# Performance work log

Measured on AMD Instinct MI355X. Metric: run time of the kernel, lower is better.

Reference implementation:

```python
import jax, jax.numpy as jnp
import numpy as np

N_QUBITS = 6
N_LAYERS = 4
N_ACTIONS = 4
PRE_DIM = 64
BATCH = 262144


def _cnot(state, ctrl, tgt):
    # state: (B, 2,...,2); flip target axis on the control=1 slice
    ca, ta = 1 + ctrl, 1 + tgt
    s0 = jnp.take(state, 0, axis=ca)
    s1 = jnp.take(state, 1, axis=ca)
    ta_in = ta if ta < ca else ta - 1
    s1 = jnp.flip(s1, axis=ta_in)
    return jnp.stack([s0, s1], axis=ca)


def _ry_batched(state, angles_q, q):
    # angles_q: (B,) per-sample RY angle on qubit q (AngleEmbedding)
    h = angles_q * 0.5
    c, s = jnp.cos(h), jnp.sin(h)
    R = jnp.stack([jnp.stack([c, -s], -1), jnp.stack([s, c], -1)], -2)  # (B,2,2)
    st = jnp.moveaxis(state, 1 + q, -1)
    st = jnp.einsum('b...i,bji->b...j', st, R)
    return jnp.moveaxis(st, -1, 1 + q)


def _ry_scalar(state, theta, q):
    h = theta * 0.5
    c, s = jnp.cos(h), jnp.sin(h)
    R = jnp.stack([jnp.stack([c, -s]), jnp.stack([s, c])])  # (2,2)
    st = jnp.moveaxis(state, 1 + q, -1)
    st = st @ R.T  # new_j = sum_i R[j,i] amp_i
    return jnp.moveaxis(st, -1, 1 + q)


def _circuit(xp, qw):
    # xp: (B, n_qubits) angles; qw: (n_layers, n_qubits)
    B = xp.shape[0]
    state = jnp.zeros((B,) + (2,) * N_QUBITS, xp.dtype)
    state = state.at[(slice(None),) + (0,) * N_QUBITS].set(1.0)
    for q in range(N_QUBITS):
        state = _ry_batched(state, xp[:, q], q)
    for l in range(N_LAYERS):
        for i in range(N_QUBITS):
            state = _cnot(state, i, (i + 1) % N_QUBITS)
        for i in range(N_QUBITS):
            state = _ry_scalar(state, qw[l, i], i)
    probs = state * state  # RY/CNOT are real; state stays real
    all_axes = tuple(range(1, N_QUBITS + 1))
    zs = []
    for q in range(N_QUBITS):
        p = jnp.sum(probs, axis=tuple(a for a in all_axes if a != 1 + q))  # (B,2)
        zs.append(p[:, 0] - p[:, 1])
    return jnp.stack(zs, -1)  # (B, n_qubits)


def setup_inputs() -> dict:
    key = jax.random.key(0)
    ks = jax.random.split(key, 10)
    x = jax.random.normal(ks[0], (BATCH, N_QUBITS), jnp.float32)
    sc = 1.0 / np.sqrt(N_QUBITS)
    W1 = jax.random.uniform(ks[1], (PRE_DIM, N_QUBITS), jnp.float32, -sc, sc)
    b1 = jax.random.uniform(ks[2], (PRE_DIM,), jnp.float32, -sc, sc)
    sc2 = 1.0 / np.sqrt(PRE_DIM)
    W2 = jax.random.uniform(ks[3], (N_QUBITS, PRE_DIM), jnp.float32, -sc2, sc2)
    b2 = jax.random.uniform(ks[4], (N_QUBITS,), jnp.float32, -sc2, sc2)
    qw = jax.random.uniform(ks[5], (N_LAYERS, N_QUBITS), jnp.float32, 0.0, 2.0 * np.pi)
    Wp = jax.random.uniform(ks[6], (N_ACTIONS, N_QUBITS), jnp.float32, -sc, sc)
    bp = jax.random.uniform(ks[7], (N_ACTIONS,), jnp.float32, -sc, sc)
    Wv = jax.random.uniform(ks[8], (1, N_QUBITS), jnp.float32, -sc, sc)
    bv = jax.random.uniform(ks[9], (1,), jnp.float32, -sc, sc)
    return {"x": x, "W1": W1, "b1": b1, "W2": W2, "b2": b2, "qw": qw,
            "Wp": Wp, "bp": bp, "Wv": Wv, "bv": bv}


def reference(x, W1, b1, W2, b2, qw, Wp, bp, Wv, bv):
    h = jax.nn.relu(x @ W1.T + b1)
    xp = jax.nn.relu(h @ W2.T + b2)          # (B, n_qubits)
    qout = _circuit(xp, qw)                   # (B, n_qubits)
    policy = jax.nn.softmax(qout @ Wp.T + bp, axis=-1)
    value = (qout @ Wv.T + bv)[:, 0]
    return policy, value
```

## Files before the change

kernel.cpp:

```cpp
#include <hip/hip_runtime.h>
#include <math.h>


#define NQ 6
#define NL 4
#define NA 4
#define PD 64
#define NS 64

__global__ __launch_bounds__(256) void qpolicy_kernel(
    const float* __restrict__ x,
    const float* __restrict__ W1,
    const float* __restrict__ b1,
    const float* __restrict__ W2,
    const float* __restrict__ b2,
    const float* __restrict__ qw,
    const float* __restrict__ Wp,
    const float* __restrict__ bp,
    const float* __restrict__ Wv,
    const float* __restrict__ bv,
    float* __restrict__ out,
    int B)
{
    const int tid = blockIdx.x * blockDim.x + threadIdx.x;

    float xi[NQ];
    {
        const float2* xv = reinterpret_cast<const float2*>(x + (size_t)tid * NQ);
        float2 a = xv[0], b = xv[1], c = xv[2];
        xi[0] = a.x; xi[1] = a.y; xi[2] = b.x; xi[3] = b.y; xi[4] = c.x; xi[5] = c.y;
    }

    float h[PD];
#pragma unroll
    for (int j = 0; j < PD; ++j) {
        float acc = b1[j];
#pragma unroll
        for (int q = 0; q < NQ; ++q) acc = fmaf(xi[q], W1[j * NQ + q], acc);
        h[j] = fmaxf(acc, 0.0f);
    }

    float xp[NQ];
#pragma unroll
    for (int i = 0; i < NQ; ++i) {
        float acc = b2[i];
#pragma unroll
        for (int j = 0; j < PD; ++j) acc = fmaf(h[j], W2[i * PD + j], acc);
        xp[i] = fmaxf(acc, 0.0f);
    }

    float cq[NQ], sq[NQ];
#pragma unroll
    for (int q = 0; q < NQ; ++q) {
        __sincosf(0.5f * xp[q], &sq[q], &cq[q]);
    }
    float st[NS];
    st[0] = 1.0f;
#pragma unroll
    for (int q = 0; q < NQ; ++q) {
        const int sz = 1 << q;
#pragma unroll
        for (int k = sz - 1; k >= 0; --k) {
            float v = st[k];
            st[2 * k]     = v * cq[q];
            st[2 * k + 1] = v * sq[q];
        }
    }

#pragma unroll
    for (int l = 0; l < NL; ++l) {
#pragma unroll
        for (int i = 0; i < NQ; ++i) {
            const int c = i, t = (i + 1) % NQ;
            const int cm = 1 << (5 - c), tm = 1 << (5 - t);
#pragma unroll
            for (int idx = 0; idx < NS; ++idx) {
                if ((idx & cm) && !(idx & tm)) {
                    float tmp = st[idx];
                    st[idx] = st[idx | tm];
                    st[idx | tm] = tmp;
                }
            }
        }
        float cw[NQ], sw[NQ];
#pragma unroll
        for (int i = 0; i < NQ; ++i) {
            __sincosf(0.5f * qw[l * NQ + i], &sw[i], &cw[i]);
        }
#pragma unroll
        for (int i = 0; i < NQ; ++i) {
            const int qm = 1 << (5 - i);
            const float c = cw[i], s = sw[i];
#pragma unroll
            for (int idx = 0; idx < NS; ++idx) {
                if (!(idx & qm)) {
                    float a0 = st[idx], a1 = st[idx | qm];
                    st[idx]      = fmaf(c, a0, -(s * a1));
                    st[idx | qm] = fmaf(c, a1,  (s * a0));
                }
            }
        }
    }

#pragma unroll
    for (int idx = 0; idx < NS; ++idx) st[idx] = st[idx] * st[idx];
    float z[NQ];
#pragma unroll
    for (int q = 0; q < NQ; ++q) {
        const int qm = 1 << (5 - q);
        float acc = 0.0f;
#pragma unroll
        for (int idx = 0; idx < NS; ++idx) {
            acc += (idx & qm) ? -st[idx] : st[idx];
        }
        z[q] = acc;
    }

    float logits[NA];
#pragma unroll
    for (int a = 0; a < NA; ++a) {
        float acc = bp[a];
#pragma unroll
        for (int q = 0; q < NQ; ++q) acc = fmaf(z[q], Wp[a * NQ + q], acc);
        logits[a] = acc;
    }
    float m = logits[0];
#pragma unroll
    for (int a = 1; a < NA; ++a) m = fmaxf(m, logits[a]);
    float e[NA];
    float esum = 0.0f;
#pragma unroll
    for (int a = 0; a < NA; ++a) { e[a] = __expf(logits[a] - m); esum += e[a]; }
    const float inv = 1.0f / esum;

    float4 pol;
    pol.x = e[0] * inv; pol.y = e[1] * inv; pol.z = e[2] * inv; pol.w = e[3] * inv;
    reinterpret_cast<float4*>(out)[tid] = pol;

    float v = bv[0];
#pragma unroll
    for (int q = 0; q < NQ; ++q) v = fmaf(z[q], Wv[q], v);
    out[(size_t)B * NA + tid] = v;
}

extern "C" void kernel_launch(void* const* d_in, const int* in_sizes, int n_in,
                              void* d_out, int out_size, void* d_ws, size_t ws_size,
                              hipStream_t stream) {
    const float* x  = (const float*)d_in[0];
    const float* W1 = (const float*)d_in[1];
    const float* b1 = (const float*)d_in[2];
    const float* W2 = (const float*)d_in[3];
    const float* b2 = (const float*)d_in[4];
    const float* qw = (const float*)d_in[5];
    const float* Wp = (const float*)d_in[6];
    const float* bp = (const float*)d_in[7];
    const float* Wv = (const float*)d_in[8];
    const float* bv = (const float*)d_in[9];
    float* out = (float*)d_out;

    const int B = in_sizes[0] / NQ;
    dim3 block(256);
    dim3 grid((B + 255) / 256);
    hipLaunchKernelGGL(qpolicy_kernel, grid, block, 0, stream,
                       x, W1, b1, W2, b2, qw, Wp, bp, Wv, bv, out, B);
}
```

Before: 104.5 us.

## Pack state as float2 pairs and use shear-decomposed rotations with packed FMA

Stores the 64-amplitude state as 32 two-float vectors so most rotations and the MLP dot products run as packed FMAs (v_pk_fma_f32). Each RY rotation becomes three shears (tan-half-angle form, with an angle shift that flips sign) instead of a 2x2 matrix multiply. The CNOT ring is remapped onto the packed layout using swaps and lane shuffles, and the Z expectations come from a tree of partial sums instead of six 64-term reductions. The goal is fewer VALU instructions per sample, at the cost of harder-to-verify index logic and slightly different rounding.

New measurement: 98.90 us. 5.3% less time.

```diff
diff --git a/kernel.cpp b/kernel.cpp
--- a/kernel.cpp
+++ b/kernel.cpp
@@ -6,7 +6,11 @@
 #define NL 4
 #define NA 4
 #define PD 64
-#define NS 64
+
+typedef float v2 __attribute__((ext_vector_type(2)));
+
+__device__ __forceinline__ v2 mk2(float a, float b) { v2 r; r.x = a; r.y = b; return r; }
+__device__ __forceinline__ v2 pkfma(v2 a, v2 b, v2 c) { return __builtin_elementwise_fma(a, b, c); }
 
 __global__ __launch_bounds__(256) void qpolicy_kernel(
     const float* __restrict__ x,
@@ -24,113 +28,173 @@
 {
     const int tid = blockIdx.x * blockDim.x + threadIdx.x;
 
-    float xi[NQ];
-    {
-        const float2* xv = reinterpret_cast<const float2*>(x + (size_t)tid * NQ);
-        float2 a = xv[0], b = xv[1], c = xv[2];
-        xi[0] = a.x; xi[1] = a.y; xi[2] = b.x; xi[3] = b.y; xi[4] = c.x; xi[5] = c.y;
-    }
-
-    float h[PD];
-#pragma unroll
-    for (int j = 0; j < PD; ++j) {
-        float acc = b1[j];
-#pragma unroll
-        for (int q = 0; q < NQ; ++q) acc = fmaf(xi[q], W1[j * NQ + q], acc);
-        h[j] = fmaxf(acc, 0.0f);
+    const v2* xv = reinterpret_cast<const v2*>(x + (size_t)tid * NQ);
+    const v2 x01 = xv[0], x23 = xv[1], x45 = xv[2];
+
+    const v2* W1v = reinterpret_cast<const v2*>(W1);
+    const v2* W2v = reinterpret_cast<const v2*>(W2);
+
+    v2 h2[PD / 2];
+#pragma unroll
+    for (int j2 = 0; j2 < PD / 2; ++j2) {
+        float hj[2];
+#pragma unroll
+        for (int u = 0; u < 2; ++u) {
+            const int j = 2 * j2 + u;
+            v2 acc = mk2(b1[j], 0.0f);
+            acc = pkfma(x01, W1v[j * 3 + 0], acc);
+            acc = pkfma(x23, W1v[j * 3 + 1], acc);
+            acc = pkfma(x45, W1v[j * 3 + 2], acc);
+            hj[u] = fmaxf(acc.x + acc.y, 0.0f);
+        }
+        h2[j2] = mk2(hj[0], hj[1]);
     }
 
     float xp[NQ];
 #pragma unroll
     for (int i = 0; i < NQ; ++i) {
-        float acc = b2[i];
-#pragma unroll
-        for (int j = 0; j < PD; ++j) acc = fmaf(h[j], W2[i * PD + j], acc);
-        xp[i] = fmaxf(acc, 0.0f);
+        v2 acc = mk2(b2[i], 0.0f);
+#pragma unroll
+        for (int k = 0; k < PD / 2; ++k) acc = pkfma(h2[k], W2v[i * (PD / 2) + k], acc);
+        xp[i] = fmaxf(acc.x + acc.y, 0.0f);
     }
 
     float cq[NQ], sq[NQ];
 #pragma unroll
-    for (int q = 0; q < NQ; ++q) {
-        __sincosf(0.5f * xp[q], &sq[q], &cq[q]);
-    }
-    float st[NS];
-    st[0] = 1.0f;
-#pragma unroll
-    for (int q = 0; q < NQ; ++q) {
+    for (int q = 0; q < NQ; ++q) __sincosf(0.5f * xp[q], &sq[q], &cq[q]);
+
+    float pr[32];
+    pr[0] = 1.0f;
+#pragma unroll
+    for (int q = 0; q < 5; ++q) {
         const int sz = 1 << q;
 #pragma unroll
         for (int k = sz - 1; k >= 0; --k) {
-            float v = st[k];
-            st[2 * k]     = v * cq[q];
-            st[2 * k + 1] = v * sq[q];
-        }
-    }
+            const float v = pr[k];
+            pr[2 * k]     = v * cq[q];
+            pr[2 * k + 1] = v * sq[q];
+        }
+    }
+    v2 st[32];
+    const v2 cs5 = mk2(cq[5], sq[5]);
+#pragma unroll
+    for (int k = 0; k < 32; ++k) st[k] = mk2(pr[k], pr[k]) * cs5;
 
 #pragma unroll
     for (int l = 0; l < NL; ++l) {
 #pragma unroll
-        for (int i = 0; i < NQ; ++i) {
-            const int c = i, t = (i + 1) % NQ;
-            const int cm = 1 << (5 - c), tm = 1 << (5 - t);
-#pragma unroll
-            for (int idx = 0; idx < NS; ++idx) {
-                if ((idx & cm) && !(idx & tm)) {
-                    float tmp = st[idx];
-                    st[idx] = st[idx | tm];
-                    st[idx | tm] = tmp;
+        for (int i = 0; i < 4; ++i) {
+            const int mc = 1 << (4 - i), mt = 1 << (3 - i);
+#pragma unroll
+            for (int k = 0; k < 32; ++k) {
+                if ((k & mc) && !(k & mt)) {
+                    v2 tmp = st[k]; st[k] = st[k | mt]; st[k | mt] = tmp;
                 }
             }
         }
-        float cw[NQ], sw[NQ];
+#pragma unroll
+        for (int k = 0; k < 32; ++k) {
+            if (k & 1) st[k] = __builtin_shufflevector(st[k], st[k], 1, 0);
+        }
+#pragma unroll
+        for (int k = 0; k < 16; ++k) {
+            const float tmp = st[k].y; st[k].y = st[k | 16].y; st[k | 16].y = tmp;
+        }
+
+        float tv[NQ], sv[NQ];
 #pragma unroll
         for (int i = 0; i < NQ; ++i) {
-            __sincosf(0.5f * qw[l * NQ + i], &sw[i], &cw[i]);
-        }
-#pragma unroll
-        for (int i = 0; i < NQ; ++i) {
-            const int qm = 1 << (5 - i);
-            const float c = cw[i], s = sw[i];
-#pragma unroll
-            for (int idx = 0; idx < NS; ++idx) {
-                if (!(idx & qm)) {
-                    float a0 = st[idx], a1 = st[idx | qm];
-                    st[idx]      = fmaf(c, a0, -(s * a1));
-                    st[idx | qm] = fmaf(c, a1,  (s * a0));
+            float hh = 0.5f * qw[l * NQ + i];
+            hh = (hh > 1.5707963f) ? (hh - 3.14159265358979f) : hh;
+            float sh, ch;
+            __sincosf(hh, &sh, &ch);
+            sv[i] = sh;
+            tv[i] = sh * __builtin_amdgcn_rcpf(1.0f + ch);
+        }
+
+#pragma unroll
+        for (int i = 0; i < 5; ++i) {
+            const int m = 1 << (4 - i);
+            const v2 vnt = mk2(-tv[i], -tv[i]);
+            const v2 vs  = mk2(sv[i], sv[i]);
+#pragma unroll
+            for (int k = 0; k < 32; ++k) {
+                if (!(k & m)) {
+                    v2 a = st[k], b = st[k | m];
+                    a = pkfma(vnt, b, a);
+                    b = pkfma(vs, a, b);
+                    a = pkfma(vnt, b, a);
+                    st[k] = a; st[k | m] = b;
                 }
             }
         }
-    }
-
-#pragma unroll
-    for (int idx = 0; idx < NS; ++idx) st[idx] = st[idx] * st[idx];
+        {
+            const float nt = -tv[5], s5 = sv[5];
+#pragma unroll
+            for (int k = 0; k < 32; ++k) {
+                float a0 = st[k].x, a1 = st[k].y;
+                a0 = fmaf(nt, a1, a0);
+                a1 = fmaf(s5, a0, a1);
+                a0 = fmaf(nt, a1, a0);
+                st[k] = mk2(a0, a1);
+            }
+        }
+    }
+
+    float a[32];
+    float S5 = 0.0f;
+#pragma unroll
+    for (int k = 0; k < 32; ++k) {
+        const v2 p = st[k] * st[k];
+        a[k] = p.x + p.y;
+        S5 += p.x;
+    }
+    float S0 = 0.0f;
+#pragma unroll
+    for (int k = 0; k < 16; ++k) S0 += a[k];
+    float b16[16];
+#pragma unroll
+    for (int k = 0; k < 16; ++k) b16[k] = a[k] + a[k | 16];
+    float S1 = 0.0f;
+#pragma unroll
+    for (int k = 0; k < 8; ++k) S1 += b16[k];
+    float b8[8];
+#pragma unroll
+    for (int k = 0; k < 8; ++k) b8[k] = b16[k] + b16[k | 8];
+    const float S2 = b8[0] + b8[1] + b8[2] + b8[3];
+    float b4[4];
+#pragma unroll
+    for (int k = 0; k < 4; ++k) b4[k] = b8[k] + b8[k | 4];
+    const float S3 = b4[0] + b4[1];
+    float b2a[2];
+    b2a[0] = b4[0] + b4[2];
+    b2a[1] = b4[1] + b4[3];
+    const float S4 = b2a[0];
+    const float T = b2a[0] + b2a[1];
+
     float z[NQ];
-#pragma unroll
-    for (int q = 0; q < NQ; ++q) {
-        const int qm = 1 << (5 - q);
-        float acc = 0.0f;
-#pragma unroll
-        for (int idx = 0; idx < NS; ++idx) {
-            acc += (idx & qm) ? -st[idx] : st[idx];
-        }
-        z[q] = acc;
-    }
+    z[0] = fmaf(2.0f, S0, -T);
+    z[1] = fmaf(2.0f, S1, -T);
+    z[2] = fmaf(2.0f, S2, -T);
+    z[3] = fmaf(2.0f, S3, -T);
+    z[4] = fmaf(2.0f, S4, -T);
+    z[5] = fmaf(2.0f, S5, -T);
 
     float logits[NA];
 #pragma unroll
-    for (int a = 0; a < NA; ++a) {
-        float acc = bp[a];
-#pragma unroll
-        for (int q = 0; q < NQ; ++q) acc = fmaf(z[q], Wp[a * NQ + q], acc);
-        logits[a] = acc;
+    for (int aidx = 0; aidx < NA; ++aidx) {
+        float acc = bp[aidx];
+#pragma unroll
+        for (int q = 0; q < NQ; ++q) acc = fmaf(z[q], Wp[aidx * NQ + q], acc);
+        logits[aidx] = acc;
     }
     float m = logits[0];
 #pragma unroll
-    for (int a = 1; a < NA; ++a) m = fmaxf(m, logits[a]);
+    for (int aidx = 1; aidx < NA; ++aidx) m = fmaxf(m, logits[aidx]);
     float e[NA];
     float esum = 0.0f;
 #pragma unroll
-    for (int a = 0; a < NA; ++a) { e[a] = __expf(logits[a] - m); esum += e[a]; }
+    for (int aidx = 0; aidx < NA; ++aidx) { e[aidx] = __expf(logits[aidx] - m); esum += e[aidx]; }
     const float inv = 1.0f / esum;
 
     float4 pol;
```
